# Kernel tuning notes

Hardware: AMD Instinct MI355X
Metric: run time of the kernel (lower is better)

Reference implementation:

```python
import jax, jax.numpy as jnp
import numpy as np

H = 128
NH = 8  # num attention heads


def _ln(x, g, b, eps=1e-5):
    m = x.mean(-1, keepdims=True)
    v = ((x - m) ** 2).mean(-1, keepdims=True)
    return (x - m) / jnp.sqrt(v + eps) * g + b


def _mha(q_in, kv_in, Wqkv, bqkv, Wo, bo):
    # torch nn.MultiheadAttention with packed in_proj, batch=1, eval (no dropout)
    h = q_in.shape[-1]
    hd = h // NH
    Wq, Wk, Wv = Wqkv[:h], Wqkv[h:2 * h], Wqkv[2 * h:]
    bq, bk, bv = bqkv[:h], bqkv[h:2 * h], bqkv[2 * h:]
    q = (q_in @ Wq.T + bq).reshape(-1, NH, hd).transpose(1, 0, 2)   # [nh, Nq, hd]
    k = (kv_in @ Wk.T + bk).reshape(-1, NH, hd).transpose(1, 0, 2)  # [nh, Nk, hd]
    v = (kv_in @ Wv.T + bv).reshape(-1, NH, hd).transpose(1, 0, 2)
    scores = jnp.einsum('hqd,hkd->hqk', q, k) / jnp.sqrt(jnp.asarray(hd, q.dtype))
    attn = jax.nn.softmax(scores, axis=-1)
    out = jnp.einsum('hqk,hkd->hqd', attn, v)                       # [nh, Nq, hd]
    out = out.transpose(1, 0, 2).reshape(-1, h)
    return out @ Wo.T + bo


def setup_inputs() -> dict:
    key = jax.random.key(0)
    ks = jax.random.split(key, 32)
    s = 0.05
    d = {
        'ligand_features': jax.random.normal(ks[0], (512, 128), jnp.float32),
        'pocket_features': jax.random.normal(ks[1], (1024, 128), jnp.float32),
        'ligand_coords': jax.random.uniform(ks[2], (512, 3), jnp.float32) * 20.0,
        'pocket_coords': jax.random.uniform(ks[3], (1024, 3), jnp.float32) * 20.0,
        # projections
        'Wl': jax.random.normal(ks[4], (H, 128), jnp.float32) * s,
        'bl': jnp.zeros((H,), jnp.float32),
        'Wp': jax.random.normal(ks[5], (H, 128), jnp.float32) * s,
        'bp': jnp.zeros((H,), jnp.float32),
        # distance encoder: 1 -> h/4 -> h/2 -> h
        'Wd1': jax.random.normal(ks[6], (H // 4, 1), jnp.float32) * s,
        'bd1': jnp.zeros((H // 4,), jnp.float32),
        'Wd2': jax.random.normal(ks[7], (H // 2, H // 4), jnp.float32) * s,
        'bd2': jnp.zeros((H // 2,), jnp.float32),
        'Wd3': jax.random.normal(ks[8], (H, H // 2), jnp.float32) * s,
        'bd3': jnp.zeros((H,), jnp.float32),
        # gates
        'Wgl': jax.random.normal(ks[9], (H, 2 * H), jnp.float32) * s,
        'bgl': jnp.zeros((H,), jnp.float32),
        'Wgp': jax.random.normal(ks[10], (H, 2 * H), jnp.float32) * s,
        'bgp': jnp.zeros((H,), jnp.float32),
        # shared cross-attention (packed qkv like torch)
        'Wqkv': jax.random.normal(ks[11], (3 * H, H), jnp.float32) * s,
        'bqkv': jnp.zeros((3 * H,), jnp.float32),
        'Wo': jax.random.normal(ks[12], (H, H), jnp.float32) * s,
        'bo': jnp.zeros((H,), jnp.float32),
        # layer norms
        'g_l': jnp.ones((H,), jnp.float32),
        'be_l': jnp.zeros((H,), jnp.float32),
        'g_p': jnp.ones((H,), jnp.float32),
        'be_p': jnp.zeros((H,), jnp.float32),
    }
    return d


def reference(ligand_features, pocket_features, ligand_coords, pocket_coords,
              Wl, bl, Wp, bp, Wd1, bd1, Wd2, bd2, Wd3, bd3,
              Wgl, bgl, Wgp, bgp, Wqkv, bqkv, Wo, bo,
              g_l, be_l, g_p, be_p):
    lig = ligand_features @ Wl.T + bl   # [Nl, H]
    poc = pocket_features @ Wp.T + bp   # [Np, H]

    # pairwise distances [Nl, Np]
    diff = ligand_coords[:, None, :] - pocket_coords[None, :, :]
    dist = jnp.sqrt(jnp.sum(diff * diff, axis=-1))

    # distance encoder MLP applied elementwise -> [Nl, Np, H]
    e = jax.nn.relu(dist[..., None] @ Wd1.T + bd1)
    e = jax.nn.relu(e @ Wd2.T + bd2)
    enc = e @ Wd3.T + bd3
    m = enc.mean(axis=-1)               # [Nl, Np]

    # ligand enhancement: softmax over pocket axis
    sw_l = jax.nn.softmax(-m, axis=-1)          # [Nl, Np]
    agg_l = sw_l @ poc                          # [Nl, H]
    gate_l = jax.nn.sigmoid(jnp.concatenate([lig, agg_l], axis=-1) @ Wgl.T + bgl)
    lig_enh = gate_l * lig + (1.0 - gate_l) * agg_l

    # pocket enhancement: transposed encoding, softmax over ligand axis
    sw_p = jax.nn.softmax(-m.T, axis=-1)        # [Np, Nl]
    agg_p = sw_p @ lig                          # [Np, H]
    gate_p = jax.nn.sigmoid(jnp.concatenate([poc, agg_p], axis=-1) @ Wgp.T + bgp)
    poc_enh = gate_p * poc + (1.0 - gate_p) * agg_p

    lig_att = _mha(lig_enh, poc_enh, Wqkv, bqkv, Wo, bo)
    poc_att = _mha(poc_enh, lig_enh, Wqkv, bqkv, Wo, bo)

    lig_fused = _ln(lig_enh + lig_att, g_l, be_l)
    poc_fused = _ln(poc_enh + poc_att, g_p, be_p)
    return (lig_fused, poc_fused)
```

## Files before the change

kernel.cpp:

```cpp
#include <hip/hip_runtime.h>
#include <math.h>

#define NL 512
#define NP 1024
#define HDIM 128

#define TAB_N 8192
#define DMAX 34.65f

#define WD3M_OFF 0
#define M_OFF    128
#define LIG_OFF  (M_OFF + NL*NP)
#define POC_OFF  (LIG_OFF + NL*HDIM)
#define LENH_OFF (POC_OFF + NP*HDIM)
#define PENH_OFF (LENH_OFF + NL*HDIM)
#define QKVL_OFF (PENH_OFF + NP*HDIM)
#define QKVP_OFF (QKVL_OFF + NL*384)
#define PARTL_OFF (QKVP_OFF + NP*384)
#define PARTP_OFF (PARTL_OFF + 512*8*8*18)
#define TAB_OFF  QKVL_OFF

__device__ __forceinline__ float dot4f(float4 a, float4 b){
  return fmaf(a.x,b.x, fmaf(a.y,b.y, fmaf(a.z,b.z, a.w*b.w)));
}

__global__ __launch_bounds__(128) void prep_kernel(const float* __restrict__ Wd3,
                                                   const float* __restrict__ bd3,
                                                   float* __restrict__ wsw){
  int t = threadIdx.x;
  if (t < 64){
    float s = 0.f;
    #pragma unroll 8
    for (int i = 0; i < 128; i++) s += Wd3[i*64 + t];
    wsw[t] = s * (1.f/128.f);
  } else if (t == 64){
    float s = 0.f;
    for (int i = 0; i < 128; i++) s += bd3[i];
    wsw[64] = s * (1.f/128.f);
  }
}

__global__ __launch_bounds__(128) void proj_kernel(const float* __restrict__ lf, const float* __restrict__ pf,
                                                   const float* __restrict__ Wl, const float* __restrict__ bl,
                                                   const float* __restrict__ Wp, const float* __restrict__ bp,
                                                   float* __restrict__ lig, float* __restrict__ poc){
  int t = threadIdx.x;
  int row0 = blockIdx.x * 4;
  const float* in; const float* W; const float* bias; float* out;
  if (row0 < NL){ in = lf + (size_t)row0*HDIM; W = Wl; bias = bl; out = lig + (size_t)row0*HDIM; }
  else { int r = row0 - NL; in = pf + (size_t)r*HDIM; W = Wp; bias = bp; out = poc + (size_t)r*HDIM; }
  __shared__ float sin[4*HDIM];
  for (int idx = t; idx < 4*HDIM; idx += 128) sin[idx] = in[idx];
  __syncthreads();
  float bv = bias[t];
  float a0 = bv, a1 = bv, a2 = bv, a3 = bv;
  const float4* wr = (const float4*)(W + (size_t)t*HDIM);
  const float4* s0 = (const float4*)(sin);
  const float4* s1 = (const float4*)(sin + HDIM);
  const float4* s2 = (const float4*)(sin + 2*HDIM);
  const float4* s3 = (const float4*)(sin + 3*HDIM);
  #pragma unroll 8
  for (int k = 0; k < 32; k++){
    float4 w = wr[k];
    a0 = fmaf(w.x, s0[k].x, fmaf(w.y, s0[k].y, fmaf(w.z, s0[k].z, fmaf(w.w, s0[k].w, a0))));
    a1 = fmaf(w.x, s1[k].x, fmaf(w.y, s1[k].y, fmaf(w.z, s1[k].z, fmaf(w.w, s1[k].w, a1))));
    a2 = fmaf(w.x, s2[k].x, fmaf(w.y, s2[k].y, fmaf(w.z, s2[k].z, fmaf(w.w, s2[k].w, a2))));
    a3 = fmaf(w.x, s3[k].x, fmaf(w.y, s3[k].y, fmaf(w.z, s3[k].z, fmaf(w.w, s3[k].w, a3))));
  }
  out[t] = a0; out[HDIM + t] = a1; out[2*HDIM + t] = a2; out[3*HDIM + t] = a3;
}

__global__ __launch_bounds__(256) void table_kernel(const float* __restrict__ Wd1, const float* __restrict__ bd1,
                                                    const float* __restrict__ Wd2, const float* __restrict__ bd2,
                                                    const float* __restrict__ wsw, float* __restrict__ tab){
  __shared__ float sWd1[32], sbd1[32], sWd2[2048], sbd2[64], swd3m[64];
  __shared__ float sbd3m;
  int t = threadIdx.x;
  int idx = blockIdx.x * 256 + t;
  if (t < 32){ sWd1[t] = Wd1[t]; sbd1[t] = bd1[t]; }
  if (t >= 32 && t < 96){ sbd2[t-32] = bd2[t-32]; swd3m[t-32] = wsw[t-32]; }
  if (t == 96) sbd3m = wsw[64];
  for (int k = t; k < 2048; k += 256) sWd2[k] = Wd2[k];
  __syncthreads();

  float d = (float)idx * (DMAX / (float)(TAB_N - 1));

  float4 e1q[8];
  const float4* w1q = (const float4*)sWd1;
  const float4* b1q = (const float4*)sbd1;
  #pragma unroll
  for (int k4 = 0; k4 < 8; k4++){
    float4 w = w1q[k4], b = b1q[k4];
    float4 e;
    e.x = fmaxf(fmaf(d, w.x, b.x), 0.f);
    e.y = fmaxf(fmaf(d, w.y, b.y), 0.f);
    e.z = fmaxf(fmaf(d, w.z, b.z), 0.f);
    e.w = fmaxf(fmaf(d, w.w, b.w), 0.f);
    e1q[k4] = e;
  }
  float mv = sbd3m;
  #pragma unroll 4
  for (int j2 = 0; j2 < 64; j2++){
    const float4* wrow = (const float4*)(sWd2 + j2*32);
    float a0 = 0.f, a1 = 0.f, a2 = 0.f, a3 = 0.f;
    #pragma unroll
    for (int k4 = 0; k4 < 8; k4++){
      float4 w = wrow[k4], e = e1q[k4];
      a0 = fmaf(w.x, e.x, a0);
      a1 = fmaf(w.y, e.y, a1);
      a2 = fmaf(w.z, e.z, a2);
      a3 = fmaf(w.w, e.w, a3);
    }
    float e2v = fmaxf(sbd2[j2] + ((a0+a1)+(a2+a3)), 0.f);
    mv = fmaf(swd3m[j2], e2v, mv);
  }
  tab[idx] = mv;
}

__global__ __launch_bounds__(1024) void agg_gate_fused(const float* __restrict__ lc, const float* __restrict__ pc,
                                                       const float* __restrict__ tab,
                                                       const float* __restrict__ lig, const float* __restrict__ poc,
                                                       const float* __restrict__ Wgl, const float* __restrict__ bgl,
                                                       const float* __restrict__ Wgp, const float* __restrict__ bgp,
                                                       float* __restrict__ lenh, float* __restrict__ penh){
  int b = blockIdx.x, t = threadIdx.x;
  bool isLig = (b < NL/4);
  int r0 = isLig ? b*4 : (b - NL/4)*4;
  int n = isLig ? NP : NL;
  const float* myFeat = isLig ? lig : poc;
  const float* otherFeat = isLig ? poc : lig;
  const float* myC = isLig ? lc : pc;
  const float* otC = isLig ? pc : lc;

  __shared__ float w[4*NP];
  __shared__ float sx[4*HDIM];
  __shared__ float sa[4*HDIM];
  __shared__ float part[8*512];
  __shared__ float gpart[4*2*128];
  __shared__ float redm[16];
  __shared__ float sgm[4], sinv[4];

  int rr = t >> 8, u = t & 255;
  int lane = t & 63, wv = t >> 6;
  int row = r0 + rr;

  if (t < 512) sx[t] = myFeat[(size_t)r0*HDIM + t];

  float cx = myC[row*3+0], cy = myC[row*3+1], cz = myC[row*3+2];
  const float inv_h = (float)(TAB_N - 1) / DMAX;
  int per = n >> 8;

  float xs[4];
  float lmax = -1e30f;
  for (int k = 0; k < per; k++){
    int j = u + (k << 8);
    float ox = otC[j*3+0], oy = otC[j*3+1], oz = otC[j*3+2];
    float dx = cx-ox, dy = cy-oy, dz = cz-oz;
    float d = sqrtf(fmaf(dx,dx, fmaf(dy,dy, dz*dz)));
    float xf = d * inv_h;
    int i0 = (int)xf;
    i0 = (i0 > TAB_N-2) ? (TAB_N-2) : i0;
    float f = xf - (float)i0;
    float v0 = tab[i0], v1 = tab[i0+1];
    xs[k] = -fmaf(f, v1 - v0, v0);
    lmax = fmaxf(lmax, xs[k]);
  }
  float v = lmax;
  #pragma unroll
  for (int off = 32; off; off >>= 1) v = fmaxf(v, __shfl_down(v, off));
  if (lane == 0) redm[wv] = v;
  __syncthreads();
  if (t < 4) sgm[t] = fmaxf(fmaxf(redm[t*4+0], redm[t*4+1]), fmaxf(redm[t*4+2], redm[t*4+3]));
  __syncthreads();
  float gm = sgm[rr];
  float lsum = 0.f;
  for (int k = 0; k < per; k++){
    float e = __expf(xs[k] - gm);
    w[rr*NP + u + (k << 8)] = e;
    lsum += e;
  }
  v = lsum;
  #pragma unroll
  for (int off = 32; off; off >>= 1) v += __shfl_down(v, off);
  if (lane == 0) redm[wv] = v;
  __syncthreads();
  if (t < 4) sinv[t] = 1.0f / ((redm[t*4+0] + redm[t*4+1]) + (redm[t*4+2] + redm[t*4+3]));
  __syncthreads();

  {
    int jg = t >> 7, cc = t & 127;
    int per2 = n >> 3;
    int jb0 = jg * per2;
    float a0 = 0.f, a1 = 0.f, a2 = 0.f, a3 = 0.f;
    #pragma unroll 4
    for (int jj = 0; jj < per2; jj++){
      int j = jb0 + jj;
      float f = otherFeat[(size_t)j*HDIM + cc];
      a0 = fmaf(w[j], f, a0);
      a1 = fmaf(w[NP + j], f, a1);
      a2 = fmaf(w[2*NP + j], f, a2);
      a3 = fmaf(w[3*NP + j], f, a3);
    }
    part[jg*512 + 0*128 + cc] = a0;
    part[jg*512 + 1*128 + cc] = a1;
    part[jg*512 + 2*128 + cc] = a2;
    part[jg*512 + 3*128 + cc] = a3;
  }
  __syncthreads();
  #pragma unroll
  for (int s = 4; s >= 1; s >>= 1){
    for (int e = t; e < s*512; e += 1024) part[e] += part[e + s*512];
    __syncthreads();
  }
  if (t < 512){
    int r = t >> 7;
    sa[t] = part[t] * sinv[r];
  }
  __syncthreads();

  {
    int r = t >> 8;
    int kg = (t >> 7) & 1;
    int col = t & 127;
    const float* Wg = isLig ? Wgl : Wgp;
    const float4* wr = (const float4*)(Wg + (size_t)col*256 + kg*128);
    const float4* inq = (kg == 0) ? (const float4*)(sx + r*128) : (const float4*)(sa + r*128);
    float g = 0.f;
    #pragma unroll 8
    for (int k = 0; k < 32; k++) g += dot4f(wr[k], inq[k]);
    gpart[r*256 + kg*128 + col] = g;
  }
  __syncthreads();
  if (t < 512){
    int r = t >> 7, c = t & 127;
    const float* bg = isLig ? bgl : bgp;
    float g = bg[c] + gpart[r*256 + c] + gpart[r*256 + 128 + c];
    g = 1.0f / (1.0f + __expf(-g));
    float xv = sx[r*128 + c], av = sa[r*128 + c];
    float* dst = isLig ? (lenh + (size_t)(r0+r)*HDIM) : (penh + (size_t)(r0+r)*HDIM);
    dst[c] = fmaf(g, xv - av, av);
  }
}

__global__ __launch_bounds__(384) void qkv_kernel(const float* __restrict__ lenh, const float* __restrict__ penh,
                                                  const float* __restrict__ Wqkv, const float* __restrict__ bqkv,
                                                  float* __restrict__ qkvl, float* __restrict__ qkvp){
  int t = threadIdx.x;
  int row0 = blockIdx.x * 4;
  const float* in; float* out; int rloc;
  if (row0 < NL){ in = lenh + (size_t)row0*HDIM; out = qkvl; rloc = row0; }
  else { rloc = row0 - NL; in = penh + (size_t)rloc*HDIM; out = qkvp; }
  __shared__ float sin[4*HDIM];
  for (int idx = t; idx < 4*HDIM; idx += 384) sin[idx] = in[idx];
  __syncthreads();
  float bv = bqkv[t];
  float a0 = bv, a1 = bv, a2 = bv, a3 = bv;
  const float4* wr = (const float4*)(Wqkv + (size_t)t*HDIM);
  const float4* s0 = (const float4*)(sin);
  const float4* s1 = (const float4*)(sin + HDIM);
  const float4* s2 = (const float4*)(sin + 2*HDIM);
  const float4* s3 = (const float4*)(sin + 3*HDIM);
  #pragma unroll 8
  for (int k = 0; k < 32; k++){
    float4 w = wr[k];
    a0 = fmaf(w.x, s0[k].x, fmaf(w.y, s0[k].y, fmaf(w.z, s0[k].z, fmaf(w.w, s0[k].w, a0))));
    a1 = fmaf(w.x, s1[k].x, fmaf(w.y, s1[k].y, fmaf(w.z, s1[k].z, fmaf(w.w, s1[k].w, a1))));
    a2 = fmaf(w.x, s2[k].x, fmaf(w.y, s2[k].y, fmaf(w.z, s2[k].z, fmaf(w.w, s2[k].w, a2))));
    a3 = fmaf(w.x, s3[k].x, fmaf(w.y, s3[k].y, fmaf(w.z, s3[k].z, fmaf(w.w, s3[k].w, a3))));
  }
  out[(size_t)(rloc+0)*384 + t] = a0;
  out[(size_t)(rloc+1)*384 + t] = a1;
  out[(size_t)(rloc+2)*384 + t] = a2;
  out[(size_t)(rloc+3)*384 + t] = a3;
}

__global__ __launch_bounds__(256) void attn_part(const float* __restrict__ qkvl, const float* __restrict__ qkvp,
                                                 float* __restrict__ partL, float* __restrict__ partP){
  int bx = blockIdx.x;
  int t = threadIdx.x;
  const float* qsrc; const float* kvsrc; int qt, slice; bool isLig;
  if (bx < 256){ isLig = true;  qt = bx >> 3; slice = bx & 7; qsrc = qkvl; kvsrc = qkvp; }
  else { int b2 = bx - 256; isLig = false; qt = b2 >> 2; slice = b2 & 3; qsrc = qkvp; kvsrc = qkvl; }
  int g = t >> 7, tt = t & 127;
  int h = tt >> 4, q = tt & 15;
  int j0 = slice*128 + g*64;

  const float4* qp = (const float4*)(qsrc + (size_t)(qt*16+q)*384 + h*16);
  float4 q0 = qp[0], q1 = qp[1], q2 = qp[2], q3 = qp[3];
  float m = -1e30f, l = 0.f;
  float4 O0 = {0,0,0,0}, O1 = {0,0,0,0}, O2 = {0,0,0,0}, O3 = {0,0,0,0};

  __shared__ float sKV[8192];
  float* myKV = sKV + g*4096;

  for (int tile = 0; tile < 4; tile++){
    int jbase = j0 + tile*16;
    __syncthreads();
    #pragma unroll
    for (int n = 0; n < 8; n++){
      int v4 = tt + n*128;
      int jj = v4 >> 6, c4 = v4 & 63;
      ((float4*)myKV)[(size_t)jj*64 + c4] = *(const float4*)(kvsrc + (size_t)(jbase+jj)*384 + 128 + c4*4);
    }
    __syncthreads();
    float s[16];
    #pragma unroll
    for (int jj = 0; jj < 16; jj++){
      const float4* kk = (const float4*)(myKV + jj*256 + h*16);
      s[jj] = (dot4f(q0, kk[0]) + dot4f(q1, kk[1]) + dot4f(q2, kk[2]) + dot4f(q3, kk[3])) * 0.25f;
    }
    float mt = s[0];
    #pragma unroll
    for (int jj = 1; jj < 16; jj++) mt = fmaxf(mt, s[jj]);
    float mn = fmaxf(m, mt);
    float corr = __expf(m - mn);
    l *= corr;
    O0.x*=corr; O0.y*=corr; O0.z*=corr; O0.w*=corr;
    O1.x*=corr; O1.y*=corr; O1.z*=corr; O1.w*=corr;
    O2.x*=corr; O2.y*=corr; O2.z*=corr; O2.w*=corr;
    O3.x*=corr; O3.y*=corr; O3.z*=corr; O3.w*=corr;
    #pragma unroll
    for (int jj = 0; jj < 16; jj++){
      float p = __expf(s[jj] - mn);
      l += p;
      const float4* vv = (const float4*)(myKV + jj*256 + 128 + h*16);
      O0.x = fmaf(p, vv[0].x, O0.x); O0.y = fmaf(p, vv[0].y, O0.y);
      O0.z = fmaf(p, vv[0].z, O0.z); O0.w = fmaf(p, vv[0].w, O0.w);
      O1.x = fmaf(p, vv[1].x, O1.x); O1.y = fmaf(p, vv[1].y, O1.y);
      O1.z = fmaf(p, vv[1].z, O1.z); O1.w = fmaf(p, vv[1].w, O1.w);
      O2.x = fmaf(p, vv[2].x, O2.x); O2.y = fmaf(p, vv[2].y, O2.y);
      O2.z = fmaf(p, vv[2].z, O2.z); O2.w = fmaf(p, vv[2].w, O2.w);
      O3.x = fmaf(p, vv[3].x, O3.x); O3.y = fmaf(p, vv[3].y, O3.y);
      O3.z = fmaf(p, vv[3].z, O3.z); O3.w = fmaf(p, vv[3].w, O3.w);
    }
    m = mn;
  }

  __syncthreads();
  float* smerge = sKV;
  if (g == 1){
    float* b = smerge + tt*19;
    b[0] = m; b[1] = l;
    b[2]=O0.x; b[3]=O0.y; b[4]=O0.z; b[5]=O0.w;
    b[6]=O1.x; b[7]=O1.y; b[8]=O1.z; b[9]=O1.w;
    b[10]=O2.x; b[11]=O2.y; b[12]=O2.z; b[13]=O2.w;
    b[14]=O3.x; b[15]=O3.y; b[16]=O3.z; b[17]=O3.w;
  }
  __syncthreads();
  if (g == 0){
    const float* b = smerge + tt*19;
    float m1 = b[0], l1 = b[1];
    float M = fmaxf(m, m1);
    float e0 = __expf(m - M), e1 = __expf(m1 - M);
    float L = l*e0 + l1*e1;
    float* dst;
    if (isLig) dst = partL + ((size_t)((qt*16+q)*8 + h)*8 + slice)*18;
    else       dst = partP + ((size_t)((qt*16+q)*8 + h)*4 + slice)*18;
    dst[0] = M; dst[1] = L;
    dst[2]  = O0.x*e0 + b[2]*e1;  dst[3]  = O0.y*e0 + b[3]*e1;
    dst[4]  = O0.z*e0 + b[4]*e1;  dst[5]  = O0.w*e0 + b[5]*e1;
    dst[6]  = O1.x*e0 + b[6]*e1;  dst[7]  = O1.y*e0 + b[7]*e1;
    dst[8]  = O1.z*e0 + b[8]*e1;  dst[9]  = O1.w*e0 + b[9]*e1;
    dst[10] = O2.x*e0 + b[10]*e1; dst[11] = O2.y*e0 + b[11]*e1;
    dst[12] = O2.z*e0 + b[12]*e1; dst[13] = O2.w*e0 + b[13]*e1;
    dst[14] = O3.x*e0 + b[14]*e1; dst[15] = O3.y*e0 + b[15]*e1;
    dst[16] = O3.z*e0 + b[16]*e1; dst[17] = O3.w*e0 + b[17]*e1;
  }
}

__global__ __launch_bounds__(128) void merge_ln(const float* __restrict__ partL, const float* __restrict__ partP,
                                                const float* __restrict__ lenh, const float* __restrict__ penh,
                                                const float* __restrict__ Wo, const float* __restrict__ bo,
                                                const float* __restrict__ g_l, const float* __restrict__ be_l,
                                                const float* __restrict__ g_p, const float* __restrict__ be_p,
                                                float* __restrict__ out){
  int r = blockIdx.x, t = threadIdx.x;
  int h = t >> 4, c = t & 15;
  int ns; const float* base;
  if (r < NL){ ns = 8; base = partL + ((size_t)(r*8 + h))*8*18; }
  else       { ns = 4; base = partP + ((size_t)((r-NL)*8 + h))*4*18; }
  float M = -1e30f;
  for (int s = 0; s < ns; s++) M = fmaxf(M, base[s*18]);
  float Lsum = 0.f, Osum = 0.f;
  for (int s = 0; s < ns; s++){
    float e = __expf(base[s*18] - M);
    Lsum = fmaf(e, base[s*18+1], Lsum);
    Osum = fmaf(e, base[s*18+2+c], Osum);
  }
  __shared__ float satt[HDIM];
  satt[t] = Osum / Lsum;
  __syncthreads();
  float o = bo[t];
  const float4* wr = (const float4*)(Wo + (size_t)t*HDIM);
  const float4* sv = (const float4*)satt;
  #pragma unroll 8
  for (int k = 0; k < 32; k++) o += dot4f(wr[k], sv[k]);
  const float* enh = (r < NL) ? (lenh + (size_t)r*HDIM) : (penh + (size_t)(r-NL)*HDIM);
  float x = enh[t] + o;
  __shared__ float red[HDIM];
  red[t] = x; __syncthreads();
  #pragma unroll
  for (int s = 64; s > 0; s >>= 1){ if (t < s) red[t] += red[t+s]; __syncthreads(); }
  float mu = red[0] * (1.f/128.f); __syncthreads();
  float dx = x - mu;
  red[t] = dx*dx; __syncthreads();
  #pragma unroll
  for (int s = 64; s > 0; s >>= 1){ if (t < s) red[t] += red[t+s]; __syncthreads(); }
  float var = red[0] * (1.f/128.f);
  float y = dx * rsqrtf(var + 1e-5f);
  if (r < NL){
    y = fmaf(y, g_l[t], be_l[t]);
    out[(size_t)r*HDIM + t] = y;
  } else {
    y = fmaf(y, g_p[t], be_p[t]);
    out[(size_t)NL*HDIM + (size_t)(r-NL)*HDIM + t] = y;
  }
}

extern "C" void kernel_launch(void* const* d_in, const int* in_sizes, int n_in,
                              void* d_out, int out_size, void* d_ws, size_t ws_size,
                              hipStream_t stream){
  const float* lf   = (const float*)d_in[0];
  const float* pf   = (const float*)d_in[1];
  const float* lc   = (const float*)d_in[2];
  const float* pc   = (const float*)d_in[3];
  const float* Wl   = (const float*)d_in[4];
  const float* bl   = (const float*)d_in[5];
  const float* Wp   = (const float*)d_in[6];
  const float* bp   = (const float*)d_in[7];
  const float* Wd1  = (const float*)d_in[8];
  const float* bd1  = (const float*)d_in[9];
  const float* Wd2  = (const float*)d_in[10];
  const float* bd2  = (const float*)d_in[11];
  const float* Wd3  = (const float*)d_in[12];
  const float* bd3  = (const float*)d_in[13];
  const float* Wgl  = (const float*)d_in[14];
  const float* bgl  = (const float*)d_in[15];
  const float* Wgp  = (const float*)d_in[16];
  const float* bgp  = (const float*)d_in[17];
  const float* Wqkv = (const float*)d_in[18];
  const float* bqkv = (const float*)d_in[19];
  const float* Wo   = (const float*)d_in[20];
  const float* bo   = (const float*)d_in[21];
  const float* g_l  = (const float*)d_in[22];
  const float* be_l = (const float*)d_in[23];
  const float* g_p  = (const float*)d_in[24];
  const float* be_p = (const float*)d_in[25];

  float* ws  = (float*)d_ws;
  float* out = (float*)d_out;
  float* wsw   = ws + WD3M_OFF;
  float* lig   = ws + LIG_OFF;
  float* poc   = ws + POC_OFF;
  float* lenh  = ws + LENH_OFF;
  float* penh  = ws + PENH_OFF;
  float* qkvl  = ws + QKVL_OFF;
  float* qkvp  = ws + QKVP_OFF;
  float* partL = ws + PARTL_OFF;
  float* partP = ws + PARTP_OFF;
  float* tab   = ws + TAB_OFF;

  prep_kernel<<<1, 128, 0, stream>>>(Wd3, bd3, wsw);
  table_kernel<<<TAB_N/256, 256, 0, stream>>>(Wd1, bd1, Wd2, bd2, wsw, tab);
  proj_kernel<<<384, 128, 0, stream>>>(lf, pf, Wl, bl, Wp, bp, lig, poc);
  agg_gate_fused<<<NL/4 + NP/4, 1024, 0, stream>>>(lc, pc, tab, lig, poc, Wgl, bgl, Wgp, bgp, lenh, penh);
  qkv_kernel<<<384, 384, 0, stream>>>(lenh, penh, Wqkv, bqkv, qkvl, qkvp);
  attn_part<<<512, 256, 0, stream>>>(qkvl, qkvp, partL, partP);
  merge_ln<<<1536, 128, 0, stream>>>(partL, partP, lenh, penh, Wo, bo, g_l, be_l, g_p, be_p, out);
}
```

Measured before the change: 232.7 us.

## Fold prep into table kernel, vectorize aggregation, read KV directly from global

Removes the separate prep kernel launch by computing the Wd3/bd3 means inside every table_kernel block. In the aggregation, each thread now accumulates float4 columns for two rows over 16 j-groups, followed by a deeper float4 shared-memory reduction. The attention kernel stops staging K/V tiles in shared memory and reads them straight from global memory through the cache, which drops several barriers. The cost is redundant mean computation in each table block and more global loads in attention.

```diff
diff --git a/kernel.cpp b/kernel.cpp
--- a/kernel.cpp
+++ b/kernel.cpp
@@ -8,7 +8,6 @@
 #define TAB_N 8192
 #define DMAX 34.65f
 
-#define WD3M_OFF 0
 #define M_OFF    128
 #define LIG_OFF  (M_OFF + NL*NP)
 #define POC_OFF  (LIG_OFF + NL*HDIM)
@@ -22,22 +21,6 @@
 
 __device__ __forceinline__ float dot4f(float4 a, float4 b){
   return fmaf(a.x,b.x, fmaf(a.y,b.y, fmaf(a.z,b.z, a.w*b.w)));
-}
-
-__global__ __launch_bounds__(128) void prep_kernel(const float* __restrict__ Wd3,
-                                                   const float* __restrict__ bd3,
-                                                   float* __restrict__ wsw){
-  int t = threadIdx.x;
-  if (t < 64){
-    float s = 0.f;
-    #pragma unroll 8
-    for (int i = 0; i < 128; i++) s += Wd3[i*64 + t];
-    wsw[t] = s * (1.f/128.f);
-  } else if (t == 64){
-    float s = 0.f;
-    for (int i = 0; i < 128; i++) s += bd3[i];
-    wsw[64] = s * (1.f/128.f);
-  }
 }
 
 __global__ __launch_bounds__(128) void proj_kernel(const float* __restrict__ lf, const float* __restrict__ pf,
@@ -72,14 +55,23 @@
 
 __global__ __launch_bounds__(256) void table_kernel(const float* __restrict__ Wd1, const float* __restrict__ bd1,
                                                     const float* __restrict__ Wd2, const float* __restrict__ bd2,
-                                                    const float* __restrict__ wsw, float* __restrict__ tab){
+                                                    const float* __restrict__ Wd3, const float* __restrict__ bd3,
+                                                    float* __restrict__ tab){
   __shared__ float sWd1[32], sbd1[32], sWd2[2048], sbd2[64], swd3m[64];
   __shared__ float sbd3m;
   int t = threadIdx.x;
   int idx = blockIdx.x * 256 + t;
-  if (t < 32){ sWd1[t] = Wd1[t]; sbd1[t] = bd1[t]; }
-  if (t >= 32 && t < 96){ sbd2[t-32] = bd2[t-32]; swd3m[t-32] = wsw[t-32]; }
-  if (t == 96) sbd3m = wsw[64];
+  if (t < 64){
+    float s = 0.f;
+    #pragma unroll 8
+    for (int i = 0; i < 128; i++) s += Wd3[i*64 + t];
+    swd3m[t] = s * (1.f/128.f);
+  } else if (t == 64){
+    float s = 0.f;
+    for (int i = 0; i < 128; i++) s += bd3[i];
+    sbd3m = s * (1.f/128.f);
+  } else if (t >= 128 && t < 160){ sWd1[t-128] = Wd1[t-128]; sbd1[t-128] = bd1[t-128]; }
+  else if (t >= 160 && t < 224){ sbd2[t-160] = bd2[t-160]; }
   for (int k = t; k < 2048; k += 256) sWd2[k] = Wd2[k];
   __syncthreads();
 
@@ -135,7 +127,7 @@
   __shared__ float w[4*NP];
   __shared__ float sx[4*HDIM];
   __shared__ float sa[4*HDIM];
-  __shared__ float part[8*512];
+  __shared__ float part[16*512];
   __shared__ float gpart[4*2*128];
   __shared__ float redm[16];
   __shared__ float sgm[4], sinv[4];
@@ -188,29 +180,43 @@
   __syncthreads();
 
   {
-    int jg = t >> 7, cc = t & 127;
-    int per2 = n >> 3;
+    int jg = t >> 6;
+    int rp = (t >> 5) & 1;
+    int c4 = t & 31;
+    int per2 = n >> 4;
     int jb0 = jg * per2;
-    float a0 = 0.f, a1 = 0.f, a2 = 0.f, a3 = 0.f;
+    int rA = rp*2, rB = rp*2 + 1;
+    const float4* of4 = (const float4*)otherFeat;
+    const float* wA = w + rA*NP;
+    const float* wB = w + rB*NP;
+    float4 accA = {0,0,0,0}, accB = {0,0,0,0};
     #pragma unroll 4
     for (int jj = 0; jj < per2; jj++){
       int j = jb0 + jj;
-      float f = otherFeat[(size_t)j*HDIM + cc];
-      a0 = fmaf(w[j], f, a0);
-      a1 = fmaf(w[NP + j], f, a1);
-      a2 = fmaf(w[2*NP + j], f, a2);
-      a3 = fmaf(w[3*NP + j], f, a3);
+      float4 f = of4[(size_t)j*32 + c4];
+      float w0 = wA[j], w1 = wB[j];
+      accA.x = fmaf(w0, f.x, accA.x); accA.y = fmaf(w0, f.y, accA.y);
+      accA.z = fmaf(w0, f.z, accA.z); accA.w = fmaf(w0, f.w, accA.w);
+      accB.x = fmaf(w1, f.x, accB.x); accB.y = fmaf(w1, f.y, accB.y);
+      accB.z = fmaf(w1, f.z, accB.z); accB.w = fmaf(w1, f.w, accB.w);
     }
-    part[jg*512 + 0*128 + cc] = a0;
-    part[jg*512 + 1*128 + cc] = a1;
-    part[jg*512 + 2*128 + cc] = a2;
-    part[jg*512 + 3*128 + cc] = a3;
-  }
-  __syncthreads();
-  #pragma unroll
-  for (int s = 4; s >= 1; s >>= 1){
-    for (int e = t; e < s*512; e += 1024) part[e] += part[e + s*512];
-    __syncthreads();
+    float4* p4 = (float4*)part;
+    p4[jg*128 + rA*32 + c4] = accA;
+    p4[jg*128 + rB*32 + c4] = accB;
+  }
+  __syncthreads();
+  {
+    float4* p4 = (float4*)part;
+    #pragma unroll
+    for (int s = 8; s >= 1; s >>= 1){
+      if (t < s*128){
+        int jg2 = t >> 7, rem = t & 127;
+        float4 a = p4[jg2*128 + rem], bb = p4[(jg2+s)*128 + rem];
+        a.x += bb.x; a.y += bb.y; a.z += bb.z; a.w += bb.w;
+        p4[jg2*128 + rem] = a;
+      }
+      __syncthreads();
+    }
   }
   if (t < 512){
     int r = t >> 7;
@@ -290,23 +296,12 @@
   float m = -1e30f, l = 0.f;
   float4 O0 = {0,0,0,0}, O1 = {0,0,0,0}, O2 = {0,0,0,0}, O3 = {0,0,0,0};
 
-  __shared__ float sKV[8192];
-  float* myKV = sKV + g*4096;
-
   for (int tile = 0; tile < 4; tile++){
     int jbase = j0 + tile*16;
-    __syncthreads();
-    #pragma unroll
-    for (int n = 0; n < 8; n++){
-      int v4 = tt + n*128;
-      int jj = v4 >> 6, c4 = v4 & 63;
-      ((float4*)myKV)[(size_t)jj*64 + c4] = *(const float4*)(kvsrc + (size_t)(jbase+jj)*384 + 128 + c4*4);
-    }
-    __syncthreads();
     float s[16];
     #pragma unroll
     for (int jj = 0; jj < 16; jj++){
-      const float4* kk = (const float4*)(myKV + jj*256 + h*16);
+      const float4* kk = (const float4*)(kvsrc + (size_t)(jbase+jj)*384 + 128 + h*16);
       s[jj] = (dot4f(q0, kk[0]) + dot4f(q1, kk[1]) + dot4f(q2, kk[2]) + dot4f(q3, kk[3])) * 0.25f;
     }
     float mt = s[0];
@@ -323,7 +318,7 @@
     for (int jj = 0; jj < 16; jj++){
       float p = __expf(s[jj] - mn);
       l += p;
-      const float4* vv = (const float4*)(myKV + jj*256 + 128 + h*16);
+      const float4* vv = (const float4*)(kvsrc + (size_t)(jbase+jj)*384 + 256 + h*16);
       O0.x = fmaf(p, vv[0].x, O0.x); O0.y = fmaf(p, vv[0].y, O0.y);
       O0.z = fmaf(p, vv[0].z, O0.z); O0.w = fmaf(p, vv[0].w, O0.w);
       O1.x = fmaf(p, vv[1].x, O1.x); O1.y = fmaf(p, vv[1].y, O1.y);
@@ -336,8 +331,8 @@
     m = mn;
   }
 
-  __syncthreads();
-  float* smerge = sKV;
+  __shared__ float smerge[128*19];
+  __syncthreads();
   if (g == 1){
     float* b = smerge + tt*19;
     b[0] = m; b[1] = l;
@@ -449,7 +444,6 @@
 
   float* ws  = (float*)d_ws;
   float* out = (float*)d_out;
-  float* wsw   = ws + WD3M_OFF;
   float* lig   = ws + LIG_OFF;
   float* poc   = ws + POC_OFF;
   float* lenh  = ws + LENH_OFF;
@@ -460,8 +454,7 @@
   float* partP = ws + PARTP_OFF;
   float* tab   = ws + TAB_OFF;
 
-  prep_kernel<<<1, 128, 0, stream>>>(Wd3, bd3, wsw);
-  table_kernel<<<TAB_N/256, 256, 0, stream>>>(Wd1, bd1, Wd2, bd2, wsw, tab);
+  table_kernel<<<TAB_N/256, 256, 0, stream>>>(Wd1, bd1, Wd2, bd2, Wd3, bd3, tab);
   proj_kernel<<<384, 128, 0, stream>>>(lf, pf, Wl, bl, Wp, bp, lig, poc);
   agg_gate_fused<<<NL/4 + NP/4, 1024, 0, stream>>>(lc, pc, tab, lig, poc, Wgl, bgl, Wgp, bgp, lenh, penh);
   qkv_kernel<<<384, 384, 0, stream>>>(lenh, penh, Wqkv, bqkv, qkvl, qkvp);
```

New measurement: 245.4 us. +5.5%, slower.
